# Kernel tuning notes

Measured on AMD Instinct MI355X. Metric: run time of the kernel, lower is better.

The kernel has to match this reference:

```python
import jax, jax.numpy as jnp
import numpy as np

DIM = 1024
GROUP = 16
N_LIN = 18   # 6 blocks * 3 quantized linears
N_LN = 5
RANK = 32
BATCH = 32768


def _dequant(q, s):
    # q: [DIM, DIM] int values in [0,16); s: [DIM*DIM/GROUP] per-group scales
    w = (q.reshape(-1, GROUP).astype(jnp.float32) - 8.0) * s[:, None]
    return w.reshape(DIM, DIM)


def _qlora_linear(x, q, s, b, la, lb):
    # x: [N, DIM]; la: [RANK, DIM]; lb: [DIM, RANK]
    w = _dequant(q, s)
    base = x @ w.T + b
    lora = (x @ la.T) @ lb.T
    return base + lora


def _layernorm(x, g, b):
    m = jnp.mean(x, axis=-1, keepdims=True)
    v = jnp.var(x, axis=-1, keepdims=True)
    return (x - m) / jnp.sqrt(v + 1e-5) * g + b


def setup_inputs() -> dict:
    key = jax.random.key(0)
    ks = jax.random.split(key, 8)
    x = jax.random.normal(ks[0], (BATCH, DIM), dtype=jnp.float32)
    wq = jax.random.randint(ks[1], (N_LIN, DIM, DIM), 0, 16, dtype=jnp.int32)
    scales = jax.random.uniform(ks[2], (N_LIN, DIM * DIM // GROUP), dtype=jnp.float32) * 0.02 + 1e-3
    bias = jax.random.normal(ks[3], (N_LIN, DIM), dtype=jnp.float32) * 0.02
    lora_a = jax.random.normal(ks[4], (N_LIN, RANK, DIM), dtype=jnp.float32) * 0.05
    lora_b = jax.random.normal(ks[5], (N_LIN, DIM, RANK), dtype=jnp.float32) * 0.05
    gamma = jnp.ones((N_LN, DIM), dtype=jnp.float32)
    beta = jnp.zeros((N_LN, DIM), dtype=jnp.float32)
    return {"x": x, "wq": wq, "scales": scales, "bias": bias,
            "lora_a": lora_a, "lora_b": lora_b, "gamma": gamma, "beta": beta}


def reference(x, wq, scales, bias, lora_a, lora_b, gamma, beta):
    h = x.astype(jnp.float32)
    li = 0
    for blk in range(6):
        r = h
        for j in range(3):
            h = _qlora_linear(h, wq[li], scales[li], bias[li], lora_a[li], lora_b[li])
            li += 1
            if j < 2:
                h = jax.nn.relu(h)
        h = h + r
        if blk < 5:
            h = _layernorm(h, gamma[blk], beta[blk])
    return h
```

## Files before the change

### kernel.cpp

```cpp
#include <hip/hip_runtime.h>

typedef unsigned int u32;
typedef unsigned short u16;
typedef _Float16 f16;
typedef f16 f16x8 __attribute__((ext_vector_type(8)));
typedef float f32x4 __attribute__((ext_vector_type(4)));
typedef u16 u16x8 __attribute__((ext_vector_type(8)));

#define DIM 1024
#define BATCH 32768
#define RANK 32
#define NLIN 18

__device__ __forceinline__ u16 f2h(float f) {
    f16 h = (f16)f;
    return *(u16*)&h;
}
__device__ __forceinline__ float h2f(u16 u) {
    f16 h;
    *(u16*)&h = u;
    return (float)h;
}

__device__ __forceinline__ void gload16(const u16* g, u16* l) {
    __builtin_amdgcn_global_load_lds((__attribute__((address_space(1))) const void*)g,
                                     (__attribute__((address_space(3))) void*)l,
                                     16, 0, 0);
}

#define BAR()        __builtin_amdgcn_s_barrier()
#define SB0()        __builtin_amdgcn_sched_barrier(0)
#define ASM_VM0()    asm volatile("s_waitcnt vmcnt(0)" ::: "memory")
#define ASM_VM4()    asm volatile("s_waitcnt vmcnt(4)" ::: "memory")
#define ASM_LG0()    asm volatile("s_waitcnt lgkmcnt(0)" ::: "memory")

__global__ __launch_bounds__(256) void build_weff(
    const int* __restrict__ wq, const float* __restrict__ scales,
    const float* __restrict__ la, const float* __restrict__ lb,
    u16* __restrict__ weff)
{
    int rb = blockIdx.x;
    int li = blockIdx.y;
    int tid = threadIdx.x;
    int row0 = rb * 16;
    __shared__ float lb_s[16][RANK];
    __shared__ float la_s[RANK][256];
    for (int idx = tid; idx < 16 * RANK; idx += 256) {
        int o = idx >> 5, r = idx & 31;
        lb_s[o][r] = lb[((size_t)li * DIM + row0 + o) * RANK + r];
    }
    const int* wqL = wq + (size_t)li * DIM * DIM;
    const float* sL = scales + (size_t)li * (DIM * DIM / 16);
    u16* wout = weff + (size_t)li * DIM * DIM;
    for (int kc = 0; kc < DIM; kc += 256) {
        __syncthreads();
        #pragma unroll
        for (int j = 0; j < 32; ++j) {
            int idx = j * 256 + tid;
            int r = idx >> 8, c = idx & 255;
            la_s[r][c] = la[((size_t)li * RANK + r) * DIM + kc + c];
        }
        __syncthreads();
        int k = kc + tid;
        for (int o = 0; o < 16; ++o) {
            int og = row0 + o;
            float acc = ((float)wqL[og * DIM + k] - 8.0f) * sL[(og << 6) + (k >> 4)];
            #pragma unroll
            for (int r = 0; r < RANK; ++r)
                acc += lb_s[o][r] * la_s[r][tid];
            wout[og * DIM + k] = f2h(acc);
        }
    }
}

__global__ __launch_bounds__(256) void xcast(const float* __restrict__ x, u16* __restrict__ o) {
    size_t i = ((size_t)blockIdx.x * 256 + threadIdx.x) * 8;
    float4 a = *(const float4*)(x + i);
    float4 b = *(const float4*)(x + i + 4);
    u16x8 v;
    v[0] = f2h(a.x); v[1] = f2h(a.y); v[2] = f2h(a.z); v[3] = f2h(a.w);
    v[4] = f2h(b.x); v[5] = f2h(b.y); v[6] = f2h(b.z); v[7] = f2h(b.w);
    *(u16x8*)(o + i) = v;
}

template<int EPI>
__global__ __launch_bounds__(512, 2) void gemm256(
    const u16* __restrict__ X, const u16* __restrict__ W,
    const float* __restrict__ bias, const u16* __restrict__ res,
    void* __restrict__ outp)
{
    __shared__ __align__(16) u16 As[2][256 * 64];
    __shared__ __align__(16) u16 Bs[2][256 * 64];
    const int tid = threadIdx.x;
    const int bid = blockIdx.x;
    const int wg = (bid & 7) * 64 + (bid >> 3);
    const int bm = wg >> 2;
    const int bn = wg & 3;
    const int wid = tid >> 6;
    const int lane = tid & 63;
    const int wm = wid >> 2;
    const int wn = wid & 3;

    const int c1 = tid, c2 = tid + 512;
    const int r1 = c1 >> 3, r2 = c2 >> 3;
    const int l1 = ((c1 & 7) ^ (r1 & 7)) * 8;
    const int l2 = ((c2 & 7) ^ (r2 & 7)) * 8;
    const u16* gA0a = X + (size_t)(bm * 256 +       r1) * DIM + l1;
    const u16* gA0b = X + (size_t)(bm * 256 +       r2) * DIM + l2;
    const u16* gA1a = X + (size_t)(bm * 256 + 128 + r1) * DIM + l1;
    const u16* gA1b = X + (size_t)(bm * 256 + 128 + r2) * DIM + l2;
    const u16* gB0a = W + (size_t)(bn * 256 +       r1) * DIM + l1;
    const u16* gB0b = W + (size_t)(bn * 256 +       r2) * DIM + l2;
    const u16* gB1a = W + (size_t)(bn * 256 + 128 + r1) * DIM + l1;
    const u16* gB1b = W + (size_t)(bn * 256 + 128 + r2) * DIM + l2;
    const int d1 = c1 * 8, d2 = c2 * 8;

    const int kg = lane >> 4;
    const int sw = lane & 7;
    const int ch0 = ((0 * 4 + kg) ^ sw) * 8;
    const int ch1 = ((1 * 4 + kg) ^ sw) * 8;
    const int aoff = (wm * 128 + (lane & 15)) * 64;
    const int boff = (wn * 64 + (lane & 15)) * 64;

    f32x4 acc[8][4];
    #pragma unroll
    for (int i = 0; i < 8; ++i)
        #pragma unroll
        for (int j = 0; j < 4; ++j)
            acc[i][j] = (f32x4){0.f, 0.f, 0.f, 0.f};
    f16x8 af[4][2];
    f16x8 bf[4][2];

    gload16(gA0a, &As[0][d1]);        gload16(gA0b, &As[0][d2]);
    gload16(gA1a, &As[0][8192 + d1]); gload16(gA1b, &As[0][8192 + d2]);
    gload16(gB0a, &Bs[0][d1]);        gload16(gB0b, &Bs[0][d2]);
    gload16(gB1a, &Bs[0][8192 + d1]); gload16(gB1b, &Bs[0][8192 + d2]);
    gload16(gB0a + 64, &Bs[1][d1]);        gload16(gB0b + 64, &Bs[1][d2]);
    gload16(gB1a + 64, &Bs[1][8192 + d1]); gload16(gB1b + 64, &Bs[1][8192 + d2]);
    gload16(gA0a + 64, &As[1][d1]);        gload16(gA0b + 64, &As[1][d2]);
    gload16(gA1a + 64, &As[1][8192 + d1]); gload16(gA1b + 64, &As[1][8192 + d2]);

    #define RD_A(MH, BUF) { \
        _Pragma("unroll") \
        for (int fm = 0; fm < 4; ++fm) { \
            af[fm][0] = *(const f16x8*)&(BUF)[aoff + ((MH)*64 + fm*16)*64 + ch0]; \
            af[fm][1] = *(const f16x8*)&(BUF)[aoff + ((MH)*64 + fm*16)*64 + ch1]; \
        } }
    #define RD_B(BUF) { \
        _Pragma("unroll") \
        for (int fn = 0; fn < 4; ++fn) { \
            bf[fn][0] = *(const f16x8*)&(BUF)[boff + (fn*16)*64 + ch0]; \
            bf[fn][1] = *(const f16x8*)&(BUF)[boff + (fn*16)*64 + ch1]; \
        } }
    #define QUAD(MH, NH) { \
        __builtin_amdgcn_s_setprio(1); \
        _Pragma("unroll") \
        for (int ks = 0; ks < 2; ++ks) \
            _Pragma("unroll") \
            for (int fm = 0; fm < 4; ++fm) \
                _Pragma("unroll") \
                for (int fn = 0; fn < 2; ++fn) \
                    acc[(MH)*4+fm][(NH)*2+fn] = __builtin_amdgcn_mfma_f32_16x16x32_f16( \
                        af[fm][ks], bf[(NH)*2+fn][ks], acc[(MH)*4+fm][(NH)*2+fn], 0, 0, 0); \
        __builtin_amdgcn_s_setprio(0); }

    asm volatile("s_waitcnt vmcnt(8)" ::: "memory");
    BAR();
    RD_A(0, (&As[0][0]));
    RD_B((&Bs[0][0]));

    #pragma unroll 1
    for (int t = 0; t < 16; ++t) {
        const int p = t & 1;
        const u16* Ap = &As[p][0];
        u16* Awr = &As[p][0];
        u16* Bwr = &Bs[p][0];
        const u16* An = &As[p ^ 1][0];
        const u16* Bn = &Bs[p ^ 1][0];
        const int ko2 = (t + 2) * 64;
        BAR();
        ASM_LG0(); SB0();
        QUAD(0, 0); QUAD(0, 1);
        RD_A(1, Ap);
        if (t <= 13) {
            gload16(gB0a + ko2, &Bwr[d1]);        gload16(gB0b + ko2, &Bwr[d2]);
            gload16(gB1a + ko2, &Bwr[8192 + d1]); gload16(gB1b + ko2, &Bwr[8192 + d2]);
        }
        SB0();
        if (t <= 13) ASM_VM4(); else if (t == 14) ASM_VM0();
        BAR();
        ASM_LG0(); SB0();
        QUAD(1, 0); QUAD(1, 1);
        if (t <= 14) {
            RD_A(0, An);
            RD_B(Bn);
        }
        if (t <= 13) {
            gload16(gA0a + ko2, &Awr[d1]);        gload16(gA0b + ko2, &Awr[d2]);
            gload16(gA1a + ko2, &Awr[8192 + d1]); gload16(gA1b + ko2, &Awr[8192 + d2]);
        }
        SB0();
    }

    ASM_LG0();
    BAR();
    float* blk = (float*)&As[0][0] + wid * 1088;
    const int mrow = bm * 256 + wm * 128;
    const int ncol = bn * 256 + wn * 64 + (lane & 7) * 8;
    float4 bv0 = *(const float4*)&bias[ncol];
    float4 bv1 = *(const float4*)&bias[ncol + 4];
    #pragma unroll
    for (int fm = 0; fm < 8; ++fm) {
        __builtin_amdgcn_sched_barrier(0);
        #pragma unroll
        for (int fn = 0; fn < 4; ++fn)
            #pragma unroll
            for (int reg = 0; reg < 4; ++reg)
                blk[((lane >> 4) * 4 + reg) * 68 + (lane & 15) + fn * 16] = acc[fm][fn][reg];
        ASM_LG0();
        __builtin_amdgcn_sched_barrier(0);
        #pragma unroll
        for (int pass = 0; pass < 2; ++pass) {
            const float* rp = &blk[(pass * 8 + (lane >> 3)) * 68 + (lane & 7) * 8];
            float4 v0 = *(const float4*)rp;
            float4 v1 = *(const float4*)(rp + 4);
            v0.x += bv0.x; v0.y += bv0.y; v0.z += bv0.z; v0.w += bv0.w;
            v1.x += bv1.x; v1.y += bv1.y; v1.z += bv1.z; v1.w += bv1.w;
            const int m = mrow + fm * 16 + pass * 8 + (lane >> 3);
            const size_t gi = (size_t)m * DIM + ncol;
            if (EPI == 0) {
                u16x8 o;
                o[0] = f2h(fmaxf(v0.x, 0.f)); o[1] = f2h(fmaxf(v0.y, 0.f));
                o[2] = f2h(fmaxf(v0.z, 0.f)); o[3] = f2h(fmaxf(v0.w, 0.f));
                o[4] = f2h(fmaxf(v1.x, 0.f)); o[5] = f2h(fmaxf(v1.y, 0.f));
                o[6] = f2h(fmaxf(v1.z, 0.f)); o[7] = f2h(fmaxf(v1.w, 0.f));
                *(u16x8*)((u16*)outp + gi) = o;
            } else {
                u16x8 rv = *(const u16x8*)(res + gi);
                v0.x += h2f(rv[0]); v0.y += h2f(rv[1]); v0.z += h2f(rv[2]); v0.w += h2f(rv[3]);
                v1.x += h2f(rv[4]); v1.y += h2f(rv[5]); v1.z += h2f(rv[6]); v1.w += h2f(rv[7]);
                if (EPI == 1) {
                    u16x8 o;
                    o[0] = f2h(v0.x); o[1] = f2h(v0.y); o[2] = f2h(v0.z); o[3] = f2h(v0.w);
                    o[4] = f2h(v1.x); o[5] = f2h(v1.y); o[6] = f2h(v1.z); o[7] = f2h(v1.w);
                    *(u16x8*)((u16*)outp + gi) = o;
                } else {
                    *(float4*)((float*)outp + gi) = v0;
                    *(float4*)((float*)outp + gi + 4) = v1;
                }
            }
        }
        ASM_LG0();
    }
    #undef RD_A
    #undef RD_B
    #undef QUAD
}

__global__ __launch_bounds__(256) void ln_k(const u16* __restrict__ in,
    const float* __restrict__ g, const float* __restrict__ b, u16* __restrict__ out)
{
    int row = blockIdx.x * 4 + (threadIdx.x >> 6);
    int lane = threadIdx.x & 63;
    const u16* rp = in + (size_t)row * DIM;
    u16x8 v0 = *(const u16x8*)(rp + lane * 8);
    u16x8 v1 = *(const u16x8*)(rp + 512 + lane * 8);
    float f[16];
    #pragma unroll
    for (int j = 0; j < 8; ++j) { f[j] = h2f(v0[j]); f[8 + j] = h2f(v1[j]); }
    float s = 0.f, sq = 0.f;
    #pragma unroll
    for (int j = 0; j < 16; ++j) { s += f[j]; sq += f[j] * f[j]; }
    #pragma unroll
    for (int m = 1; m < 64; m <<= 1) { s += __shfl_xor(s, m); sq += __shfl_xor(sq, m); }
    float mean = s * (1.0f / 1024.0f);
    float var = sq * (1.0f / 1024.0f) - mean * mean;
    float rstd = 1.0f / sqrtf(var + 1e-5f);
    u16x8 o0, o1;
    #pragma unroll
    for (int j = 0; j < 8; ++j) {
        int c0 = lane * 8 + j, c1 = 512 + lane * 8 + j;
        o0[j] = f2h((f[j] - mean) * rstd * g[c0] + b[c0]);
        o1[j] = f2h((f[8 + j] - mean) * rstd * g[c1] + b[c1]);
    }
    u16* op = out + (size_t)row * DIM;
    *(u16x8*)(op + lane * 8) = o0;
    *(u16x8*)(op + 512 + lane * 8) = o1;
}

extern "C" void kernel_launch(void* const* d_in, const int* in_sizes, int n_in,
                              void* d_out, int out_size, void* d_ws, size_t ws_size,
                              hipStream_t stream) {
    const float* x      = (const float*)d_in[0];
    const int*   wq     = (const int*)d_in[1];
    const float* scales = (const float*)d_in[2];
    const float* bias   = (const float*)d_in[3];
    const float* la     = (const float*)d_in[4];
    const float* lb     = (const float*)d_in[5];
    const float* gamma  = (const float*)d_in[6];
    const float* beta   = (const float*)d_in[7];

    char* ws = (char*)d_ws;
    u16* Weff = (u16*)ws;
    u16* actA = (u16*)(ws + (size_t)NLIN * DIM * DIM * 2);
    u16* actB = actA + (size_t)BATCH * DIM;
    u16* dob  = (u16*)d_out;
    float* dof = (float*)d_out;

    build_weff<<<dim3(64, 18), 256, 0, stream>>>(wq, scales, la, lb, Weff);
    xcast<<<(BATCH * DIM) / 2048, 256, 0, stream>>>(x, actA);

    int li = 0;
    for (int blk = 0; blk < 6; ++blk) {
        const u16* w0 = Weff + (size_t)(li + 0) * DIM * DIM;
        const u16* w1 = Weff + (size_t)(li + 1) * DIM * DIM;
        const u16* w2 = Weff + (size_t)(li + 2) * DIM * DIM;
        const float* b0 = bias + (li + 0) * DIM;
        const float* b1 = bias + (li + 1) * DIM;
        const float* b2 = bias + (li + 2) * DIM;
        if (blk < 5) {
            gemm256<0><<<512, 512, 0, stream>>>(actA, w0, b0, nullptr, actB);
            gemm256<0><<<512, 512, 0, stream>>>(actB, w1, b1, nullptr, dob);
            gemm256<1><<<512, 512, 0, stream>>>(dob,  w2, b2, actA, actB);
            ln_k<<<BATCH / 4, 256, 0, stream>>>(actB, gamma + blk * DIM, beta + blk * DIM, actA);
        } else {
            gemm256<0><<<512, 512, 0, stream>>>(actA, w0, b0, nullptr, dob);
            gemm256<0><<<512, 512, 0, stream>>>(dob,  w1, b1, nullptr, actB);
            gemm256<2><<<512, 512, 0, stream>>>(actB, w2, b2, actA, (void*)dof);
        }
        li += 3;
    }
}
```

Baseline: 1.421 ms.

## Triple-buffer A tiles in GEMM and keep LoRA-A in registers in build_weff

The GEMM's A operand goes from a double buffer to a rotating triple buffer. A-tile loads for step t+2 are now issued at the start of each iteration, and B loads move to after the mid-iteration barrier. This is meant to issue global-to-LDS copies earlier and cut barrier stalls, at the cost of more LDS (160KB total) and changed vmcnt wait semantics. build_weff drops its shared-memory staging: each thread keeps its LoRA-A column in registers and computes four output rows at a time, reading LoRA-B directly from global memory.

```diff
diff --git a/kernel.cpp b/kernel.cpp
--- a/kernel.cpp
+++ b/kernel.cpp
@@ -32,6 +32,7 @@
 #define SB0()        __builtin_amdgcn_sched_barrier(0)
 #define ASM_VM0()    asm volatile("s_waitcnt vmcnt(0)" ::: "memory")
 #define ASM_VM4()    asm volatile("s_waitcnt vmcnt(4)" ::: "memory")
+#define ASM_VM8()    asm volatile("s_waitcnt vmcnt(8)" ::: "memory")
 #define ASM_LG0()    asm volatile("s_waitcnt lgkmcnt(0)" ::: "memory")
 
 __global__ __launch_bounds__(256) void build_weff(
@@ -39,36 +40,41 @@
     const float* __restrict__ la, const float* __restrict__ lb,
     u16* __restrict__ weff)
 {
-    int rb = blockIdx.x;
-    int li = blockIdx.y;
-    int tid = threadIdx.x;
-    int row0 = rb * 16;
-    __shared__ float lb_s[16][RANK];
-    __shared__ float la_s[RANK][256];
-    for (int idx = tid; idx < 16 * RANK; idx += 256) {
-        int o = idx >> 5, r = idx & 31;
-        lb_s[o][r] = lb[((size_t)li * DIM + row0 + o) * RANK + r];
-    }
+    const int rb = blockIdx.x;
+    const int li = blockIdx.y;
+    const int tid = threadIdx.x;
+    const int row0 = rb * 16;
     const int* wqL = wq + (size_t)li * DIM * DIM;
     const float* sL = scales + (size_t)li * (DIM * DIM / 16);
+    const float* laL = la + (size_t)li * RANK * DIM;
+    const float* lbL = lb + (size_t)li * DIM * RANK;
     u16* wout = weff + (size_t)li * DIM * DIM;
-    for (int kc = 0; kc < DIM; kc += 256) {
-        __syncthreads();
-        #pragma unroll
-        for (int j = 0; j < 32; ++j) {
-            int idx = j * 256 + tid;
-            int r = idx >> 8, c = idx & 255;
-            la_s[r][c] = la[((size_t)li * RANK + r) * DIM + kc + c];
-        }
-        __syncthreads();
-        int k = kc + tid;
-        for (int o = 0; o < 16; ++o) {
-            int og = row0 + o;
-            float acc = ((float)wqL[og * DIM + k] - 8.0f) * sL[(og << 6) + (k >> 4)];
+
+    for (int kc = 0; kc < 4; ++kc) {
+        const int k = kc * 256 + tid;
+        float lar[RANK];
+        #pragma unroll
+        for (int r = 0; r < RANK; ++r) lar[r] = laL[r * DIM + k];
+        const int ks = k >> 4;
+        #pragma unroll
+        for (int og = 0; og < 16; og += 4) {
+            const int m0 = row0 + og;
+            float a0 = ((float)wqL[(m0 + 0) * DIM + k] - 8.0f) * sL[((m0 + 0) << 6) + ks];
+            float a1 = ((float)wqL[(m0 + 1) * DIM + k] - 8.0f) * sL[((m0 + 1) << 6) + ks];
+            float a2 = ((float)wqL[(m0 + 2) * DIM + k] - 8.0f) * sL[((m0 + 2) << 6) + ks];
+            float a3 = ((float)wqL[(m0 + 3) * DIM + k] - 8.0f) * sL[((m0 + 3) << 6) + ks];
             #pragma unroll
-            for (int r = 0; r < RANK; ++r)
-                acc += lb_s[o][r] * la_s[r][tid];
-            wout[og * DIM + k] = f2h(acc);
+            for (int r = 0; r < RANK; ++r) {
+                const float lv = lar[r];
+                a0 += lbL[(m0 + 0) * RANK + r] * lv;
+                a1 += lbL[(m0 + 1) * RANK + r] * lv;
+                a2 += lbL[(m0 + 2) * RANK + r] * lv;
+                a3 += lbL[(m0 + 3) * RANK + r] * lv;
+            }
+            wout[(m0 + 0) * DIM + k] = f2h(a0);
+            wout[(m0 + 1) * DIM + k] = f2h(a1);
+            wout[(m0 + 2) * DIM + k] = f2h(a2);
+            wout[(m0 + 3) * DIM + k] = f2h(a3);
         }
     }
 }
@@ -89,8 +95,8 @@
     const float* __restrict__ bias, const u16* __restrict__ res,
     void* __restrict__ outp)
 {
-    __shared__ __align__(16) u16 As[2][256 * 64];
-    __shared__ __align__(16) u16 Bs[2][256 * 64];
+    __shared__ __align__(16) u16 As3[3 * 16384];
+    __shared__ __align__(16) u16 Bs[2 * 16384];
     const int tid = threadIdx.x;
     const int bid = blockIdx.x;
     const int wg = (bid & 7) * 64 + (bid >> 3);
@@ -131,14 +137,14 @@
     f16x8 af[4][2];
     f16x8 bf[4][2];
 
-    gload16(gA0a, &As[0][d1]);        gload16(gA0b, &As[0][d2]);
-    gload16(gA1a, &As[0][8192 + d1]); gload16(gA1b, &As[0][8192 + d2]);
-    gload16(gB0a, &Bs[0][d1]);        gload16(gB0b, &Bs[0][d2]);
-    gload16(gB1a, &Bs[0][8192 + d1]); gload16(gB1b, &Bs[0][8192 + d2]);
-    gload16(gB0a + 64, &Bs[1][d1]);        gload16(gB0b + 64, &Bs[1][d2]);
-    gload16(gB1a + 64, &Bs[1][8192 + d1]); gload16(gB1b + 64, &Bs[1][8192 + d2]);
-    gload16(gA0a + 64, &As[1][d1]);        gload16(gA0b + 64, &As[1][d2]);
-    gload16(gA1a + 64, &As[1][8192 + d1]); gload16(gA1b + 64, &As[1][8192 + d2]);
+    gload16(gA0a, &As3[d1]);        gload16(gA0b, &As3[d2]);
+    gload16(gA1a, &As3[8192 + d1]); gload16(gA1b, &As3[8192 + d2]);
+    gload16(gB0a, &Bs[d1]);         gload16(gB0b, &Bs[d2]);
+    gload16(gB1a, &Bs[8192 + d1]);  gload16(gB1b, &Bs[8192 + d2]);
+    gload16(gA0a + 64, &As3[16384 + d1]);        gload16(gA0b + 64, &As3[16384 + d2]);
+    gload16(gA1a + 64, &As3[16384 + 8192 + d1]); gload16(gA1b + 64, &As3[16384 + 8192 + d2]);
+    gload16(gB0a + 64, &Bs[16384 + d1]);         gload16(gB0b + 64, &Bs[16384 + d2]);
+    gload16(gB1a + 64, &Bs[16384 + 8192 + d1]);  gload16(gB1b + 64, &Bs[16384 + 8192 + d2]);
 
     #define RD_A(MH, BUF) { \
         _Pragma("unroll") \
@@ -164,47 +170,41 @@
                         af[fm][ks], bf[(NH)*2+fn][ks], acc[(MH)*4+fm][(NH)*2+fn], 0, 0, 0); \
         __builtin_amdgcn_s_setprio(0); }
 
-    asm volatile("s_waitcnt vmcnt(8)" ::: "memory");
+    ASM_VM8();
     BAR();
-    RD_A(0, (&As[0][0]));
-    RD_B((&Bs[0][0]));
-
+    RD_A(0, (&As3[0]));
+    RD_B((&Bs[0]));
+
+    int aCur = 0, aNext = 16384, aWr = 32768;
+    int bCur = 0, bNext = 16384;
     #pragma unroll 1
     for (int t = 0; t < 16; ++t) {
-        const int p = t & 1;
-        const u16* Ap = &As[p][0];
-        u16* Awr = &As[p][0];
-        u16* Bwr = &Bs[p][0];
-        const u16* An = &As[p ^ 1][0];
-        const u16* Bn = &Bs[p ^ 1][0];
         const int ko2 = (t + 2) * 64;
-        BAR();
+        if (t <= 13) {
+            gload16(gA0a + ko2, &As3[aWr + d1]);        gload16(gA0b + ko2, &As3[aWr + d2]);
+            gload16(gA1a + ko2, &As3[aWr + 8192 + d1]); gload16(gA1b + ko2, &As3[aWr + 8192 + d2]);
+        }
         ASM_LG0(); SB0();
         QUAD(0, 0); QUAD(0, 1);
-        RD_A(1, Ap);
-        if (t <= 13) {
-            gload16(gB0a + ko2, &Bwr[d1]);        gload16(gB0b + ko2, &Bwr[d2]);
-            gload16(gB1a + ko2, &Bwr[8192 + d1]); gload16(gB1b + ko2, &Bwr[8192 + d2]);
-        }
-        SB0();
+        RD_A(1, (&As3[aCur]));
         if (t <= 13) ASM_VM4(); else if (t == 14) ASM_VM0();
         BAR();
+        if (t <= 13) {
+            gload16(gB0a + ko2, &Bs[bCur + d1]);        gload16(gB0b + ko2, &Bs[bCur + d2]);
+            gload16(gB1a + ko2, &Bs[bCur + 8192 + d1]); gload16(gB1b + ko2, &Bs[bCur + 8192 + d2]);
+        }
         ASM_LG0(); SB0();
         QUAD(1, 0); QUAD(1, 1);
         if (t <= 14) {
-            RD_A(0, An);
-            RD_B(Bn);
-        }
-        if (t <= 13) {
-            gload16(gA0a + ko2, &Awr[d1]);        gload16(gA0b + ko2, &Awr[d2]);
-            gload16(gA1a + ko2, &Awr[8192 + d1]); gload16(gA1b + ko2, &Awr[8192 + d2]);
-        }
-        SB0();
-    }
-
-    ASM_LG0();
-    BAR();
-    float* blk = (float*)&As[0][0] + wid * 1088;
+            RD_A(0, (&As3[aNext]));
+            RD_B((&Bs[bNext]));
+        }
+        BAR();
+        int tmp = aCur; aCur = aNext; aNext = aWr; aWr = tmp;
+        tmp = bCur; bCur = bNext; bNext = tmp;
+    }
+
+    float* blk = (float*)&As3[0] + wid * 1088;
     const int mrow = bm * 256 + wm * 128;
     const int ncol = bn * 256 + wn * 64 + (lane & 7) * 8;
     float4 bv0 = *(const float4*)&bias[ncol];
```

After: 1.467 ms. 3.2% more time.
